# Kernel optimization log

Measured on AMD Instinct MI355X. Metric: run time of the kernel, lower is better.

## Reference

```python
import jax, jax.numpy as jnp
import numpy as np

B, S, HID = 1, 4096, 2048
H, KVH, D = 8, 4, 256
QR, KR, VR = 6, 2, 2
WINDOW = 1024
SOFTCAP = 50.0
SCALING = 256.0 ** -0.5  # query_pre_attn_scalar ** -0.5
EPS = 1e-6
NEG = -2.3819763e38


def _rope(x, cos, sin):
    # x: [B,S,R,D]; cos/sin: [S,D//2] -> rotate interleaved complex pairs
    xr = x.reshape(*x.shape[:-1], D // 2, 2)
    x1, x2 = xr[..., 0], xr[..., 1]
    c = cos[None, :, None, :]
    s = sin[None, :, None, :]
    out = jnp.stack([x1 * c - x2 * s, x1 * s + x2 * c], axis=-1)
    return out.reshape(x.shape)


def _rmsnorm(x, w):
    var = jnp.mean(x * x, axis=-1, keepdims=True)
    return x * jax.lax.rsqrt(var + EPS) * (1.0 + w)


def setup_inputs() -> dict:
    key = jax.random.key(0)
    ks = jax.random.split(key, 12)
    sc = HID ** -0.5
    pos = np.arange(S, dtype=np.float32)
    inv = 1.0 / (10000.0 ** (np.arange(0, D, 2, dtype=np.float32) / D))
    fr = pos[:, None] * inv[None, :]
    return {
        'hidden_states': jax.random.normal(ks[0], (B, S, HID), jnp.float32),
        'freqs_cos': jnp.asarray(np.cos(fr), jnp.float32),
        'freqs_sin': jnp.asarray(np.sin(fr), jnp.float32),
        'W_A_q': jax.random.normal(ks[1], (H * QR, HID), jnp.float32) * sc,
        'W_A_k': jax.random.normal(ks[2], (KVH * KR, HID), jnp.float32) * sc,
        'W_A_v': jax.random.normal(ks[3], (KVH * VR, HID), jnp.float32) * sc,
        'W_B_q': jax.random.normal(ks[4], (QR * D, HID), jnp.float32) * sc,
        'W_B_k': jax.random.normal(ks[5], (KR * D, HID), jnp.float32) * sc,
        'W_B_v': jax.random.normal(ks[6], (VR * D, HID), jnp.float32) * sc,
        'W_o': jax.random.normal(ks[7], (HID, H * D), jnp.float32) * (H * D) ** -0.5,
        'q_norm_w': jnp.zeros((D,), jnp.float32),
        'k_norm_w': jnp.zeros((D,), jnp.float32),
        'k_cache_A': jnp.zeros((B, S, KVH, KR), jnp.float32),
        'k_cache_B': jnp.zeros((B, S, KR, D), jnp.float32),
        'v_cache_A': jnp.zeros((B, S, KVH, VR), jnp.float32),
        'v_cache_B': jnp.zeros((B, S, VR, D), jnp.float32),
        'kv_write_indices': jnp.arange(S, dtype=jnp.int32),
    }


def reference(hidden_states, freqs_cos, freqs_sin, W_A_q, W_A_k, W_A_v,
              W_B_q, W_B_k, W_B_v, W_o, q_norm_w, k_norm_w,
              k_cache_A, k_cache_B, v_cache_A, v_cache_B, kv_write_indices):
    x = hidden_states  # [B,S,HID]
    # factorized projections
    A_q = (x @ W_A_q.T).reshape(B, S, H, QR)
    A_k = (x @ W_A_k.T).reshape(B, S, KVH, KR)
    A_v = (x @ W_A_v.T).reshape(B, S, KVH, VR)
    B_q = (x @ W_B_q.T).reshape(B, S, QR, D)
    B_k = (x @ W_B_k.T).reshape(B, S, KR, D)
    B_v = (x @ W_B_v.T).reshape(B, S, VR, D)
    # RoPE on head-dim factors of Q and K
    B_q = _rope(B_q, freqs_cos, freqs_sin)
    B_k = _rope(B_k, freqs_cos, freqs_sin)
    # write factors into the TPA KV cache
    k_cache_A = k_cache_A.at[:, kv_write_indices].set(A_k)
    k_cache_B = k_cache_B.at[:, kv_write_indices].set(B_k)
    v_cache_A = v_cache_A.at[:, kv_write_indices].set(A_v)
    v_cache_B = v_cache_B.at[:, kv_write_indices].set(B_v)
    # reconstruct Q/K/V from rank-R tensor products (mean over rank)
    q = jnp.einsum('bshr,bsrd->bshd', A_q, B_q) / QR          # [B,S,H,D]
    k = jnp.einsum('btkr,btrd->btkd', k_cache_A, k_cache_B) / KR  # [B,T,KVH,D]
    v = jnp.einsum('btkr,btrd->btkd', v_cache_A, v_cache_B) / VR
    # QK RMSNorm
    q = _rmsnorm(q, q_norm_w)
    k = _rmsnorm(k, k_norm_w)
    # GQA: expand KV heads to query heads
    rep = H // KVH
    k = jnp.repeat(k, rep, axis=2)  # [B,T,H,D]
    v = jnp.repeat(v, rep, axis=2)
    # scores with softcapping + sliding-window causal mask
    scores = jnp.einsum('bshd,bthd->bhst', q * SCALING, k)
    scores = jnp.tanh(scores / SOFTCAP) * SOFTCAP
    q_pos = kv_write_indices[:, None]        # [S,1]
    k_pos = jnp.arange(S, dtype=jnp.int32)[None, :]  # [1,T]
    diff = q_pos - k_pos
    allowed = (diff >= 0) & (diff < WINDOW)
    scores = jnp.where(allowed[None, None], scores, NEG)
    probs = jax.nn.softmax(scores, axis=-1)
    out = jnp.einsum('bhst,bthd->bshd', probs, v).reshape(B, S, H * D)
    return out @ W_o.T
```

## Files before the change

### kernel.cpp

```cpp
#include <hip/hip_runtime.h>
#include <hip/hip_bf16.h>
#include <cstdint>
#include <cstddef>

constexpr int SEQ   = 4096;
constexpr int HIDN  = 2048;
constexpr int NHEAD = 8;
constexpr int NKVH  = 4;
constexpr int DH    = 256;
constexpr int NPROJ = 2624;
constexpr int NPROJP= 2688;
constexpr int WIN   = 1024;

typedef __attribute__((ext_vector_type(4))) float f32x4;
typedef __attribute__((ext_vector_type(8))) short bf16x8;
typedef unsigned short u16;

__device__ __forceinline__ u16 f2bf(float x) {
  union { float f; uint32_t u; } v; v.f = x;
  uint32_t r = v.u + 0x7fffu + ((v.u >> 16) & 1u);
  return (u16)(r >> 16);
}

__device__ __forceinline__ uint32_t cvtpk(float lo, float hi) {
  uint32_t r;
  asm("v_cvt_pk_bf16_f32 %0, %1, %2" : "=v"(r) : "v"(lo), "v"(hi));
  return r;
}

__device__ __forceinline__ void gl_lds16(const u16* g, u16* l) {
  __builtin_amdgcn_global_load_lds(
      (const __attribute__((address_space(1))) uint32_t*)g,
      (__attribute__((address_space(3))) uint32_t*)l, 16, 0, 0);
}

__device__ __forceinline__ void sync_vm() {
  asm volatile("s_waitcnt vmcnt(0)" ::: "memory");
  __builtin_amdgcn_s_barrier();
  __builtin_amdgcn_sched_barrier(0);
}

__global__ __launch_bounds__(256) void k_cvt(const float* __restrict__ src,
                                             u16* __restrict__ dst, int n4) {
  int i = blockIdx.x * 256 + threadIdx.x;
  if (i >= n4) return;
  float4 v = ((const float4*)src)[i];
  ushort4 o; o.x = f2bf(v.x); o.y = f2bf(v.y); o.z = f2bf(v.z); o.w = f2bf(v.w);
  ((ushort4*)dst)[i] = o;
}

__global__ __launch_bounds__(256) void k_wcat(
    const float* __restrict__ waq, const float* __restrict__ wak,
    const float* __restrict__ wav, const float* __restrict__ wbq,
    const float* __restrict__ wbk, const float* __restrict__ wbv,
    u16* __restrict__ wcat) {
  const int r = blockIdx.x;
  const int col0 = threadIdx.x * 8;
  u16* out = wcat + (size_t)r * HIDN + col0;
  const float* src = nullptr; int rr = 0;
  if      (r < 48)   { src = waq; rr = r; }
  else if (r < 56)   { src = wak; rr = r - 48; }
  else if (r < 64)   { src = wav; rr = r - 56; }
  else if (r < 1600) { src = wbq; rr = r - 64; }
  else if (r < 2112) { src = wbk; rr = r - 1600; }
  else if (r < 2624) { src = wbv; rr = r - 2112; }
  if (!src) {
    ushort4 z = {0,0,0,0}; ((ushort4*)out)[0] = z; ((ushort4*)out)[1] = z; return;
  }
  const float* s = src + (size_t)rr * HIDN + col0;
#pragma unroll
  for (int i = 0; i < 2; ++i) {
    float4 v = ((const float4*)s)[i];
    ushort4 o; o.x = f2bf(v.x); o.y = f2bf(v.y); o.z = f2bf(v.z); o.w = f2bf(v.w);
    ((ushort4*)out)[i] = o;
  }
}

__global__ __launch_bounds__(256)
void k_gemm_bt(const u16* __restrict__ A, const u16* __restrict__ Bm,
               float* __restrict__ C, int M, int N, int K) {
  __shared__ u16 lA[2][128 * 32];
  __shared__ u16 lB[2][128 * 32];
  const int tid = threadIdx.x;
  const int wid = tid >> 6, lane = tid & 63;
  const int l15 = lane & 15, g = lane >> 4;
  const int m0 = blockIdx.y * 128, n0 = blockIdx.x * 128;
  const int wr = wid >> 1, wc = wid & 1;
  f32x4 acc[4][4];
#pragma unroll
  for (int m = 0; m < 4; ++m)
#pragma unroll
    for (int n = 0; n < 4; ++n) acc[m][n] = (f32x4){0.f,0.f,0.f,0.f};
  const int NT = K >> 5;

  auto stage = [&](int buf, int kt) {
    const int k0 = kt << 5;
#pragma unroll
    for (int i = 0; i < 2; ++i) {
      const int u = i * 256 + tid;
      const int row = u >> 2, cs = u & 3;
      const int cc = cs ^ ((row >> 1) & 3);
      gl_lds16(A  + (size_t)(m0 + row) * K + k0 + cc * 8, &lA[buf][(i*256 + wid*64) * 8]);
      gl_lds16(Bm + (size_t)(n0 + row) * K + k0 + cc * 8, &lB[buf][(i*256 + wid*64) * 8]);
    }
  };

  stage(0, 0);
  int cur = 0;
  for (int kt = 0; kt < NT; ++kt) {
    __syncthreads();
    if (kt + 1 < NT) stage(cur ^ 1, kt + 1);
    bf16x8 af[4], bfr[4];
#pragma unroll
    for (int m = 0; m < 4; ++m) {
      const int row = wr*64 + m*16 + l15;
      const int cc = g ^ ((row >> 1) & 3);
      af[m] = *(const bf16x8*)&lA[cur][row*32 + cc*8];
    }
#pragma unroll
    for (int n = 0; n < 4; ++n) {
      const int row = wc*64 + n*16 + l15;
      const int cc = g ^ ((row >> 1) & 3);
      bfr[n] = *(const bf16x8*)&lB[cur][row*32 + cc*8];
    }
#pragma unroll
    for (int m = 0; m < 4; ++m)
#pragma unroll
      for (int n = 0; n < 4; ++n)
        acc[m][n] = __builtin_amdgcn_mfma_f32_16x16x32_bf16(af[m], bfr[n], acc[m][n], 0, 0, 0);
    cur ^= 1;
  }
#pragma unroll
  for (int m = 0; m < 4; ++m)
#pragma unroll
    for (int n = 0; n < 4; ++n)
#pragma unroll
      for (int j = 0; j < 4; ++j) {
        const int row = m0 + wr*64 + m*16 + g*4 + j;
        const int col = n0 + wc*64 + n*16 + l15;
        C[(size_t)row * N + col] = acc[m][n][j];
      }
}

__global__ __launch_bounds__(256)
void k_qkv(const float* __restrict__ Y, const float* __restrict__ cosT,
           const float* __restrict__ sinT, const float* __restrict__ qw,
           const float* __restrict__ kw, u16* __restrict__ q_s,
           u16* __restrict__ k_s, u16* __restrict__ v_s) {
  const int s = blockIdx.x;
  const int d = threadIdx.x;
  __shared__ float row[NPROJ];
  __shared__ float red[12][4];
  const float* yr = Y + (size_t)s * NPROJP;
  for (int u = d; u < NPROJ; u += 256) row[u] = yr[u];
  __syncthreads();
  const int i = d >> 1;
  const float cf = cosT[s * 128 + i];
  const float sf = sinT[s * 128 + i];
  const bool odd = d & 1;
  float bq[6], bk[2], bv[2];
#pragma unroll
  for (int r = 0; r < 6; ++r) {
    float x1 = row[64 + r*256 + 2*i], x2 = row[64 + r*256 + 2*i + 1];
    bq[r] = odd ? (x1*sf + x2*cf) : (x1*cf - x2*sf);
  }
#pragma unroll
  for (int r = 0; r < 2; ++r) {
    float x1 = row[1600 + r*256 + 2*i], x2 = row[1600 + r*256 + 2*i + 1];
    bk[r] = odd ? (x1*sf + x2*cf) : (x1*cf - x2*sf);
    bv[r] = row[2112 + r*256 + d];
  }
  float qv[8], kv[4], vv[4];
#pragma unroll
  for (int h = 0; h < 8; ++h) {
    float a = 0.f;
#pragma unroll
    for (int r = 0; r < 6; ++r) a += row[h*6 + r] * bq[r];
    qv[h] = a * (1.0f / 6.0f);
  }
#pragma unroll
  for (int c = 0; c < 4; ++c) {
    kv[c] = (row[48 + c*2]*bk[0] + row[48 + c*2 + 1]*bk[1]) * 0.5f;
    vv[c] = (row[56 + c*2]*bv[0] + row[56 + c*2 + 1]*bv[1]) * 0.5f;
  }
  const int lane = d & 63, wv = d >> 6;
#pragma unroll
  for (int t = 0; t < 12; ++t) {
    float x = (t < 8) ? qv[t] : kv[t - 8];
    float ss = x * x;
#pragma unroll
    for (int off = 32; off > 0; off >>= 1) ss += __shfl_xor(ss, off);
    if (lane == 0) red[t][wv] = ss;
  }
  __syncthreads();
  const float qwf = 1.0f + qw[d], kwf = 1.0f + kw[d];
#pragma unroll
  for (int h = 0; h < 8; ++h) {
    float v = red[h][0] + red[h][1] + red[h][2] + red[h][3];
    float r = rsqrtf(v * (1.0f/256.0f) + 1e-6f);
    q_s[((size_t)s*8 + h)*256 + d] = f2bf(qv[h] * r * qwf * 0.0625f);
  }
#pragma unroll
  for (int c = 0; c < 4; ++c) {
    float v = red[8+c][0] + red[8+c][1] + red[8+c][2] + red[8+c][3];
    float r = rsqrtf(v * (1.0f/256.0f) + 1e-6f);
    k_s[((size_t)s*4 + c)*256 + d] = f2bf(kv[c] * r * kwf);
    v_s[((size_t)s*4 + c)*256 + d] = f2bf(vv[c]);
  }
}

__global__ __launch_bounds__(256)
void k_vt(const u16* __restrict__ v_s, u16* __restrict__ vT) {
  __shared__ u16 tile[64][72];
  const int s0 = blockIdx.x * 64, d0 = blockIdx.y * 64, c = blockIdx.z;
  const int tid = threadIdx.x;
#pragma unroll
  for (int it = 0; it < 2; ++it) {
    const int u = it * 256 + tid;
    const int r = u >> 3, cc = u & 7;
    const u16* s = &v_s[(((size_t)(s0 + r))*4 + c)*256 + d0 + cc*8];
    ushort4 a = *(const ushort4*)s, b = *(const ushort4*)(s + 4);
    tile[r][cc*8+0]=a.x; tile[r][cc*8+1]=a.y; tile[r][cc*8+2]=a.z; tile[r][cc*8+3]=a.w;
    tile[r][cc*8+4]=b.x; tile[r][cc*8+5]=b.y; tile[r][cc*8+6]=b.z; tile[r][cc*8+7]=b.w;
  }
  __syncthreads();
#pragma unroll
  for (int it = 0; it < 2; ++it) {
    const int u = it * 256 + tid;
    const int dr = u >> 3, sc = u & 7;
    ushort4 a, b;
    a.x = tile[sc*8+0][dr]; a.y = tile[sc*8+1][dr]; a.z = tile[sc*8+2][dr]; a.w = tile[sc*8+3][dr];
    b.x = tile[sc*8+4][dr]; b.y = tile[sc*8+5][dr]; b.z = tile[sc*8+6][dr]; b.w = tile[sc*8+7][dr];
    u16* o = vT + ((size_t)c*256 + d0 + dr)*SEQ + s0 + sc*8;
    *(ushort4*)o = a; *(ushort4*)(o + 4) = b;
  }
}

__global__ __launch_bounds__(256)
void k_attn(const u16* __restrict__ q_s, const u16* __restrict__ k_s,
            const u16* __restrict__ vT, const int* __restrict__ idx,
            u16* __restrict__ ao) {
  __shared__ u16 Kt[2][32 * 256];
  __shared__ u16 Vt[2][256 * 32];
  __shared__ u16 Pb[4][16 * 40];
  const int b = blockIdx.x;
  const int c = b & 3, qt = b >> 2;
  const int q0 = qt * 32;
  const int tid = threadIdx.x;
  const int wid = tid >> 6, lane = tid & 63;
  const int l15 = lane & 15, g = lane >> 4;
  const int h = 2*c + (wid >> 1);
  const int qsub = wid & 1;
  const int qrow = q0 + qsub*16 + l15;
  const int qpos = idx[qrow];

  bf16x8 qf[8];
  const u16* qb = q_s + ((size_t)qrow * 8 + h) * 256;
#pragma unroll
  for (int kk = 0; kk < 8; ++kk) qf[kk] = *(const bf16x8*)(qb + kk*32 + g*8);

  int kbase[8];
#pragma unroll
  for (int kk = 0; kk < 8; ++kk)
    kbase[kk] = l15*256 + (((4*kk + g) ^ (l15 & 7)) * 8);
  const int vbase = l15*32 + ((g ^ ((l15 >> 1) & 3)) * 8);
  u16* KtF = &Kt[0][0];
  u16* VtF = &Vt[0][0];
  u16* Pw  = &Pb[wid][0];

  f32x4 accO[16];
#pragma unroll
  for (int n = 0; n < 16; ++n) accO[n] = (f32x4){0.f,0.f,0.f,0.f};
  float mrun = -50.0f, lrun = 0.0f;

  int t0 = q0 - (WIN - 1); if (t0 < 0) t0 = 0;
  const int kt_lo = t0 >> 5, kt_hi = qt;

  const int srow = tid >> 5;
  const int scl  = (tid & 31) ^ srow;
  const int vdr  = tid >> 2;
  const int vlc  = (tid & 3) ^ ((tid >> 3) & 3);
  const u16* kg = k_s + (size_t)(kt_lo*32 + srow) * 1024 + c*256 + scl*8;
  const u16* vg = vT  + (size_t)c*1048576 + (size_t)vdr*4096 + kt_lo*32 + vlc*8;

  auto stage = [&](int buf) {
#pragma unroll
    for (int i = 0; i < 4; ++i)
      gl_lds16(kg + i*8192,   &Kt[buf][(i*256 + wid*64) * 8]);
#pragma unroll
    for (int i = 0; i < 4; ++i)
      gl_lds16(vg + i*262144, &Vt[buf][(i*256 + wid*64) * 8]);
  };

  stage(0);
  int cur = 0;
  for (int kt = kt_lo; kt <= kt_hi; ++kt) {
    const int k0 = kt * 32;
    sync_vm();
    if (kt < kt_hi) { kg += 32768; vg += 32; stage(cur ^ 1); }

    const int kco = cur * 8192;
    f32x4 s0 = (f32x4){0.f,0.f,0.f,0.f}, s1 = (f32x4){0.f,0.f,0.f,0.f};
#pragma unroll
    for (int kk = 0; kk < 8; ++kk) {
      bf16x8 kf0 = *(const bf16x8*)&KtF[kbase[kk] + kco];
      bf16x8 kf1 = *(const bf16x8*)&KtF[kbase[kk] + kco + 4096];
      s0 = __builtin_amdgcn_mfma_f32_16x16x32_bf16(kf0, qf[kk], s0, 0, 0, 0);
      s1 = __builtin_amdgcn_mfma_f32_16x16x32_bf16(kf1, qf[kk], s1, 0, 0, 0);
    }

    float tv[8];
#pragma unroll
    for (int nk = 0; nk < 2; ++nk)
#pragma unroll
      for (int j = 0; j < 4; ++j) {
        float x = (nk == 0) ? s0[j] : s1[j];
        float u = exp2f(x * 0.05770780163555854f);
        tv[nk*4+j] = fmaf(-100.0f, __builtin_amdgcn_rcpf(1.0f + u), 50.0f);
      }
    const int dbase = qpos - k0;
    if (kt == kt_hi) {
#pragma unroll
      for (int nk = 0; nk < 2; ++nk)
#pragma unroll
        for (int j = 0; j < 4; ++j)
          if (nk*16 + g*4 + j > dbase) tv[nk*4+j] = -1e38f;
    } else if (k0 < q0 - 992) {
#pragma unroll
      for (int nk = 0; nk < 2; ++nk)
#pragma unroll
        for (int j = 0; j < 4; ++j)
          if (dbase - (nk*16 + g*4 + j) > 1023) tv[nk*4+j] = -1e38f;
    }

    float tmax = tv[0];
#pragma unroll
    for (int t = 1; t < 8; ++t) tmax = fmaxf(tmax, tv[t]);
    tmax = fmaxf(tmax, __shfl_xor(tmax, 16));
    tmax = fmaxf(tmax, __shfl_xor(tmax, 32));
    if (__any(tmax > mrun + 8.0f)) {
      const float mnew = fmaxf(mrun, tmax);
      const float scale = exp2f((mrun - mnew) * 1.442695041f);
      float scj[4];
#pragma unroll
      for (int j = 0; j < 4; ++j) scj[j] = __shfl(scale, g*4 + j);
#pragma unroll
      for (int n = 0; n < 16; ++n) {
        accO[n][0] *= scj[0]; accO[n][1] *= scj[1];
        accO[n][2] *= scj[2]; accO[n][3] *= scj[3];
      }
      lrun *= scale;
      mrun = mnew;
    }
    const float mr2 = mrun * 1.442695041f;
    float p[8], psum = 0.0f;
#pragma unroll
    for (int t = 0; t < 8; ++t) {
      p[t] = exp2f(fmaf(tv[t], 1.442695041f, -mr2));
      psum += p[t];
    }
    psum += __shfl_xor(psum, 16);
    psum += __shfl_xor(psum, 32);
    lrun += psum;

    uint32_t a0 = cvtpk(p[0], p[1]), a1 = cvtpk(p[2], p[3]);
    uint32_t b0 = cvtpk(p[4], p[5]), b1 = cvtpk(p[6], p[7]);
    { uint2 w = {a0, a1}; *(uint2*)&Pw[l15*40 + g*4]      = w; }
    { uint2 w = {b0, b1}; *(uint2*)&Pw[l15*40 + 16 + g*4] = w; }
    bf16x8 pa = *(const bf16x8*)&Pw[l15*40 + g*8];
    const int vco = cur * 8192;
#pragma unroll
    for (int n = 0; n < 16; ++n) {
      bf16x8 vf = *(const bf16x8*)&VtF[vbase + vco + n*512];
      accO[n] = __builtin_amdgcn_mfma_f32_16x16x32_bf16(pa, vf, accO[n], 0, 0, 0);
    }
    cur ^= 1;
  }

  const float linv = 1.0f / lrun;
  float lj[4];
#pragma unroll
  for (int j = 0; j < 4; ++j) lj[j] = __shfl(linv, g*4 + j);
#pragma unroll
  for (int n = 0; n < 16; ++n)
#pragma unroll
    for (int j = 0; j < 4; ++j) {
      const int r = q0 + qsub*16 + g*4 + j;
      ao[(size_t)r * HIDN + h*256 + n*16 + l15] = f2bf(accO[n][j] * lj[j]);
    }
}

extern "C" void kernel_launch(void* const* d_in, const int* in_sizes, int n_in,
                              void* d_out, int out_size, void* d_ws, size_t ws_size,
                              hipStream_t stream) {
  const float* x    = (const float*)d_in[0];
  const float* fcos = (const float*)d_in[1];
  const float* fsin = (const float*)d_in[2];
  const float* waq  = (const float*)d_in[3];
  const float* wak  = (const float*)d_in[4];
  const float* wav  = (const float*)d_in[5];
  const float* wbq  = (const float*)d_in[6];
  const float* wbk  = (const float*)d_in[7];
  const float* wbv  = (const float*)d_in[8];
  const float* wo   = (const float*)d_in[9];
  const float* qnw  = (const float*)d_in[10];
  const float* knw  = (const float*)d_in[11];
  const int*   idx  = (const int*)d_in[16];
  float* out = (float*)d_out;

  char* p = (char*)d_ws;
  u16*  xb   = (u16*)p;                 p += (size_t)SEQ*HIDN*2;
  u16*  wcat = (u16*)p;                 p += (size_t)NPROJP*HIDN*2;
  u16*  wob  = (u16*)p;                 p += (size_t)HIDN*HIDN*2;
  float* ypr = (float*)p;               p += (size_t)SEQ*NPROJP*4;
  u16*  q_s  = (u16*)p;                 p += (size_t)SEQ*NHEAD*DH*2;
  u16*  k_s  = (u16*)p;                 p += (size_t)SEQ*NKVH*DH*2;
  u16*  v_s  = (u16*)p;                 p += (size_t)SEQ*NKVH*DH*2;
  u16*  vT   = (u16*)p;                 p += (size_t)SEQ*NKVH*DH*2;
  u16*  ao   = (u16*)p;                 p += (size_t)SEQ*HIDN*2;

  k_cvt <<<(SEQ*HIDN/4 + 255)/256, 256, 0, stream>>>(x, xb, SEQ*HIDN/4);
  k_cvt <<<(HIDN*HIDN/4 + 255)/256, 256, 0, stream>>>(wo, wob, HIDN*HIDN/4);
  k_wcat<<<NPROJP, 256, 0, stream>>>(waq, wak, wav, wbq, wbk, wbv, wcat);
  k_gemm_bt<<<dim3(NPROJP/128, SEQ/128), 256, 0, stream>>>(xb, wcat, ypr, SEQ, NPROJP, HIDN);
  k_qkv <<<SEQ, 256, 0, stream>>>(ypr, fcos, fsin, qnw, knw, q_s, k_s, v_s);
  k_vt  <<<dim3(SEQ/64, DH/64, NKVH), 256, 0, stream>>>(v_s, vT);
  k_attn<<<dim3(SEQ/32 * NKVH), 256, 0, stream>>>(q_s, k_s, vT, idx, ao);
  k_gemm_bt<<<dim3(HIDN/128, SEQ/128), 256, 0, stream>>>(ao, wob, out, SEQ, HIDN, HIDN);
}
```

Baseline: 253.7 us.

## Store projection output as bf16, swizzle GEMM tiles by XCD, tune attention softmax

The projection GEMM now writes bf16 instead of fp32, roughly halving the intermediate buffer traffic between the GEMM and the QKV kernel. GEMM workgroups are remapped so that neighbouring tiles land on the same XCD, which should improve L2 reuse. Both GEMM and attention raise wave priority around their MFMA blocks with s_setprio. The attention softmax uses raw exp2 and rcp intrinsics, and it defers the cross-lane row-sum reduction to the end and does the max reduction only when a rescale is triggered. Rounding the projection output to bf16 costs some precision before RoPE and RMSNorm.

Result: faster. 224.7 us (-11.4%).

```diff
diff --git a/kernel.cpp b/kernel.cpp
--- a/kernel.cpp
+++ b/kernel.cpp
@@ -21,6 +21,9 @@
   uint32_t r = v.u + 0x7fffu + ((v.u >> 16) & 1u);
   return (u16)(r >> 16);
 }
+__device__ __forceinline__ float bf2f(u16 v) {
+  union { uint32_t u; float f; } w; w.u = (uint32_t)v << 16; return w.f;
+}
 
 __device__ __forceinline__ uint32_t cvtpk(float lo, float hi) {
   uint32_t r;
@@ -38,6 +41,12 @@
   asm volatile("s_waitcnt vmcnt(0)" ::: "memory");
   __builtin_amdgcn_s_barrier();
   __builtin_amdgcn_sched_barrier(0);
+}
+
+__device__ __forceinline__ int xcd_swz(int wg, int nwg) {
+  const int q = nwg >> 3, r = nwg & 7;
+  const int xcd = wg & 7, lo = wg >> 3;
+  return (xcd < r ? xcd * (q + 1) : r * (q + 1) + (xcd - r) * q) + lo;
 }
 
 __global__ __launch_bounds__(256) void k_cvt(const float* __restrict__ src,
@@ -76,15 +85,18 @@
   }
 }
 
+template<int OBF16>
 __global__ __launch_bounds__(256)
 void k_gemm_bt(const u16* __restrict__ A, const u16* __restrict__ Bm,
-               float* __restrict__ C, int M, int N, int K) {
+               void* __restrict__ Cv, int M, int N, int K) {
   __shared__ u16 lA[2][128 * 32];
   __shared__ u16 lB[2][128 * 32];
   const int tid = threadIdx.x;
   const int wid = tid >> 6, lane = tid & 63;
   const int l15 = lane & 15, g = lane >> 4;
-  const int m0 = blockIdx.y * 128, n0 = blockIdx.x * 128;
+  const int nwg = gridDim.x * gridDim.y;
+  int wg = xcd_swz(blockIdx.y * gridDim.x + blockIdx.x, nwg);
+  const int m0 = (wg / gridDim.x) * 128, n0 = (wg % gridDim.x) * 128;
   const int wr = wid >> 1, wc = wid & 1;
   f32x4 acc[4][4];
 #pragma unroll
@@ -123,11 +135,13 @@
       const int cc = g ^ ((row >> 1) & 3);
       bfr[n] = *(const bf16x8*)&lB[cur][row*32 + cc*8];
     }
+    __builtin_amdgcn_s_setprio(1);
 #pragma unroll
     for (int m = 0; m < 4; ++m)
 #pragma unroll
       for (int n = 0; n < 4; ++n)
         acc[m][n] = __builtin_amdgcn_mfma_f32_16x16x32_bf16(af[m], bfr[n], acc[m][n], 0, 0, 0);
+    __builtin_amdgcn_s_setprio(0);
     cur ^= 1;
   }
 #pragma unroll
@@ -138,12 +152,13 @@
       for (int j = 0; j < 4; ++j) {
         const int row = m0 + wr*64 + m*16 + g*4 + j;
         const int col = n0 + wc*64 + n*16 + l15;
-        C[(size_t)row * N + col] = acc[m][n][j];
+        if constexpr (OBF16) ((u16*)Cv)[(size_t)row * N + col] = f2bf(acc[m][n][j]);
+        else                 ((float*)Cv)[(size_t)row * N + col] = acc[m][n][j];
       }
 }
 
 __global__ __launch_bounds__(256)
-void k_qkv(const float* __restrict__ Y, const float* __restrict__ cosT,
+void k_qkv(const u16* __restrict__ Y, const float* __restrict__ cosT,
            const float* __restrict__ sinT, const float* __restrict__ qw,
            const float* __restrict__ kw, u16* __restrict__ q_s,
            u16* __restrict__ k_s, u16* __restrict__ v_s) {
@@ -151,8 +166,12 @@
   const int d = threadIdx.x;
   __shared__ float row[NPROJ];
   __shared__ float red[12][4];
-  const float* yr = Y + (size_t)s * NPROJP;
-  for (int u = d; u < NPROJ; u += 256) row[u] = yr[u];
+  const u16* yr = Y + (size_t)s * NPROJP;
+  for (int u4 = d; u4 < NPROJ/4; u4 += 256) {
+    ushort4 v4 = ((const ushort4*)yr)[u4];
+    row[u4*4+0] = bf2f(v4.x); row[u4*4+1] = bf2f(v4.y);
+    row[u4*4+2] = bf2f(v4.z); row[u4*4+3] = bf2f(v4.w);
+  }
   __syncthreads();
   const int i = d >> 1;
   const float cf = cosT[s * 128 + i];
@@ -301,6 +320,7 @@
 
     const int kco = cur * 8192;
     f32x4 s0 = (f32x4){0.f,0.f,0.f,0.f}, s1 = (f32x4){0.f,0.f,0.f,0.f};
+    __builtin_amdgcn_s_setprio(1);
 #pragma unroll
     for (int kk = 0; kk < 8; ++kk) {
       bf16x8 kf0 = *(const bf16x8*)&KtF[kbase[kk] + kco];
@@ -308,6 +328,7 @@
       s0 = __builtin_amdgcn_mfma_f32_16x16x32_bf16(kf0, qf[kk], s0, 0, 0, 0);
       s1 = __builtin_amdgcn_mfma_f32_16x16x32_bf16(kf1, qf[kk], s1, 0, 0, 0);
     }
+    __builtin_amdgcn_s_setprio(0);
 
     float tv[8];
 #pragma unroll
@@ -315,7 +336,7 @@
 #pragma unroll
       for (int j = 0; j < 4; ++j) {
         float x = (nk == 0) ? s0[j] : s1[j];
-        float u = exp2f(x * 0.05770780163555854f);
+        float u = __builtin_amdgcn_exp2f(x * 0.05770780163555854f);
         tv[nk*4+j] = fmaf(-100.0f, __builtin_amdgcn_rcpf(1.0f + u), 50.0f);
       }
     const int dbase = qpos - k0;
@@ -336,11 +357,11 @@
     float tmax = tv[0];
 #pragma unroll
     for (int t = 1; t < 8; ++t) tmax = fmaxf(tmax, tv[t]);
-    tmax = fmaxf(tmax, __shfl_xor(tmax, 16));
-    tmax = fmaxf(tmax, __shfl_xor(tmax, 32));
     if (__any(tmax > mrun + 8.0f)) {
-      const float mnew = fmaxf(mrun, tmax);
-      const float scale = exp2f((mrun - mnew) * 1.442695041f);
+      float tq = fmaxf(tmax, __shfl_xor(tmax, 16));
+      tq = fmaxf(tq, __shfl_xor(tq, 32));
+      const float mnew = fmaxf(mrun, tq);
+      const float scale = __builtin_amdgcn_exp2f((mrun - mnew) * 1.442695041f);
       float scj[4];
 #pragma unroll
       for (int j = 0; j < 4; ++j) scj[j] = __shfl(scale, g*4 + j);
@@ -353,15 +374,12 @@
       mrun = mnew;
     }
     const float mr2 = mrun * 1.442695041f;
-    float p[8], psum = 0.0f;
+    float p[8];
 #pragma unroll
     for (int t = 0; t < 8; ++t) {
-      p[t] = exp2f(fmaf(tv[t], 1.442695041f, -mr2));
-      psum += p[t];
-    }
-    psum += __shfl_xor(psum, 16);
-    psum += __shfl_xor(psum, 32);
-    lrun += psum;
+      p[t] = __builtin_amdgcn_exp2f(fmaf(tv[t], 1.442695041f, -mr2));
+      lrun += p[t];
+    }
 
     uint32_t a0 = cvtpk(p[0], p[1]), a1 = cvtpk(p[2], p[3]);
     uint32_t b0 = cvtpk(p[4], p[5]), b1 = cvtpk(p[6], p[7]);
@@ -369,15 +387,19 @@
     { uint2 w = {b0, b1}; *(uint2*)&Pw[l15*40 + 16 + g*4] = w; }
     bf16x8 pa = *(const bf16x8*)&Pw[l15*40 + g*8];
     const int vco = cur * 8192;
+    __builtin_amdgcn_s_setprio(1);
 #pragma unroll
     for (int n = 0; n < 16; ++n) {
       bf16x8 vf = *(const bf16x8*)&VtF[vbase + vco + n*512];
       accO[n] = __builtin_amdgcn_mfma_f32_16x16x32_bf16(pa, vf, accO[n], 0, 0, 0);
     }
+    __builtin_amdgcn_s_setprio(0);
     cur ^= 1;
   }
 
-  const float linv = 1.0f / lrun;
+  lrun += __shfl_xor(lrun, 16);
+  lrun += __shfl_xor(lrun, 32);
+  const float linv = __builtin_amdgcn_rcpf(lrun);
   float lj[4];
 #pragma unroll
   for (int j = 0; j < 4; ++j) lj[j] = __shfl(linv, g*4 + j);
@@ -412,7 +434,7 @@
   u16*  xb   = (u16*)p;                 p += (size_t)SEQ*HIDN*2;
   u16*  wcat = (u16*)p;                 p += (size_t)NPROJP*HIDN*2;
   u16*  wob  = (u16*)p;                 p += (size_t)HIDN*HIDN*2;
-  float* ypr = (float*)p;               p += (size_t)SEQ*NPROJP*4;
+  u16*  ypr  = (u16*)p;                 p += (size_t)SEQ*NPROJP*2;
   u16*  q_s  = (u16*)p;                 p += (size_t)SEQ*NHEAD*DH*2;
   u16*  k_s  = (u16*)p;                 p += (size_t)SEQ*NKVH*DH*2;
   u16*  v_s  = (u16*)p;                 p += (size_t)SEQ*NKVH*DH*2;
@@ -422,9 +444,9 @@
   k_cvt <<<(SEQ*HIDN/4 + 255)/256, 256, 0, stream>>>(x, xb, SEQ*HIDN/4);
   k_cvt <<<(HIDN*HIDN/4 + 255)/256, 256, 0, stream>>>(wo, wob, HIDN*HIDN/4);
   k_wcat<<<NPROJP, 256, 0, stream>>>(waq, wak, wav, wbq, wbk, wbv, wcat);
-  k_gemm_bt<<<dim3(NPROJP/128, SEQ/128), 256, 0, stream>>>(xb, wcat, ypr, SEQ, NPROJP, HIDN);
+  k_gemm_bt<1><<<dim3(NPROJP/128, SEQ/128), 256, 0, stream>>>(xb, wcat, ypr, SEQ, NPROJP, HIDN);
   k_qkv <<<SEQ, 256, 0, stream>>>(ypr, fcos, fsin, qnw, knw, q_s, k_s, v_s);
   k_vt  <<<dim3(SEQ/64, DH/64, NKVH), 256, 0, stream>>>(v_s, vT);
   k_attn<<<dim3(SEQ/32 * NKVH), 256, 0, stream>>>(q_s, k_s, vT, idx, ao);
-  k_gemm_bt<<<dim3(HIDN/128, SEQ/128), 256, 0, stream>>>(ao, wob, out, SEQ, HIDN, HIDN);
-}
+  k_gemm_bt<0><<<dim3(HIDN/128, SEQ/128), 256, 0, stream>>>(ao, wob, out, SEQ, HIDN, HIDN);
+}
```
